# Kernel tuning notes

Hardware: AMD Instinct MI355X
Metric: run time of the kernel (lower is better)

## Reference

```python
import jax, jax.numpy as jnp
import numpy as np

N, E, F, H, G = 50000, 640000, 128, 128, 64


def setup_inputs() -> dict:
    key = jax.random.key(0)
    ks = jax.random.split(key, 10)
    x = jax.random.normal(ks[0], (N, F), dtype=jnp.float32)
    edge_index = jax.random.randint(ks[1], (2, E), 0, N)
    batch = jnp.sort(jax.random.randint(ks[2], (N,), 0, G))

    def glorot(k, shp):
        return jax.random.normal(k, shp, dtype=jnp.float32) * np.float32(1.0 / np.sqrt(shp[0]))

    W1 = glorot(ks[3], (F, H)); b1 = jnp.zeros((H,), jnp.float32)
    W2 = glorot(ks[4], (H, H)); b2 = jnp.zeros((H,), jnp.float32)
    W3 = glorot(ks[5], (H, H)); b3 = jnp.zeros((H,), jnp.float32)
    W4 = glorot(ks[6], (H, 2)); b4 = jnp.zeros((2,), jnp.float32)
    return {"x": x, "W1": W1, "b1": b1, "W2": W2, "b2": b2,
            "W3": W3, "b3": b3, "W4": W4, "b4": b4,
            "edge_index": edge_index, "batch": batch, "num_graphs": G}


def reference(x, W1, b1, W2, b2, W3, b3, W4, b4, edge_index, batch, num_graphs):
    n = x.shape[0]
    loop = jnp.arange(n, dtype=edge_index.dtype)
    src = jnp.concatenate([edge_index[0], loop])  # with self-loops (PyG GCNConv default)
    dst = jnp.concatenate([edge_index[1], loop])
    # symmetric degree normalization: D^{-1/2} (A+I) D^{-1/2}
    deg = jax.ops.segment_sum(jnp.ones_like(src, dtype=x.dtype), dst, num_segments=n)
    dinv = jnp.where(deg > 0, jax.lax.rsqrt(deg), 0.0)
    norm = (dinv[src] * dinv[dst])[:, None]  # [E+N, 1]

    def gcn_conv(h, W, b):
        m = h @ W                                   # transform first (F->H), then propagate
        agg = jax.ops.segment_sum(m[src] * norm, dst, num_segments=n)
        return agg + b

    h = jax.nn.relu(gcn_conv(x, W1, b1))
    h = jax.nn.relu(gcn_conv(h, W2, b2))
    g = jax.ops.segment_max(h, batch, num_segments=num_graphs)  # global_max_pool
    z = jax.nn.relu(g @ W3 + b3)                    # dropout is identity in eval
    logits = z @ W4 + b4
    return jax.nn.log_softmax(logits, axis=1)
```

## Files before the change

kernel.cpp:

```cpp
#include <hip/hip_runtime.h>
#include <hip/hip_bf16.h>
#include <math.h>

#define HDIM 128
#define SCAN_B 256
#define NBLK 256

typedef short bfrag __attribute__((ext_vector_type(8)));
typedef float f32x4 __attribute__((ext_vector_type(4)));

__device__ inline unsigned short f2bf_rne(float x) {
    unsigned u = __float_as_uint(x);
    u = (u + 0x7fffu + ((u >> 16) & 1u)) >> 16;
    return (unsigned short)u;
}
__device__ inline float bf_lo(unsigned u) { return __uint_as_float(u << 16); }
__device__ inline float bf_hi(unsigned u) { return __uint_as_float(u & 0xffff0000u); }
__device__ inline unsigned bf_pack(float lo, float hi) {
    return ((unsigned)f2bf_rne(hi) << 16) | (unsigned)f2bf_rne(lo);
}


__device__ inline void hist_body(int b, const int* __restrict__ dst,
                                 int* __restrict__ hist, int E, int chunk, int nbuck) {
    __shared__ int hl[256];
    int t = threadIdx.x;
    hl[t] = 0;
    __syncthreads();
    int start = b * chunk, end = min(E, start + chunk);
    for (int e = start + t; e < end; e += 256) atomicAdd(&hl[dst[e] >> 8], 1);
    __syncthreads();
    if (t < nbuck) hist[t * NBLK + b] = hl[t];
}

__device__ inline void wfrag_body(int b, const float* __restrict__ W1,
                                  const float* __restrict__ W2,
                                  unsigned short* __restrict__ w1h,
                                  unsigned short* __restrict__ w1l,
                                  unsigned short* __restrict__ w2h,
                                  unsigned short* __restrict__ w2l) {
    const float* W = (b < 64) ? W1 : W2;
    unsigned short* whi = (b < 64) ? w1h : w2h;
    unsigned short* wlo = (b < 64) ? w1l : w2l;
    int idx = (b & 63) * 256 + threadIdx.x;
    int k = idx >> 7;
    int n = idx & 127;
    int kt = k >> 5, q = (k >> 3) & 3, j = k & 7;
    int lm = n >> 3, nt = n & 7;
    int lane = q * 16 + lm;
    int o = ((kt * 8 + nt) * 64 + lane) * 8 + j;
    float x = W[idx];
    unsigned short hb = f2bf_rne(x);
    float hf = __uint_as_float(((unsigned)hb) << 16);
    unsigned short lb = f2bf_rne(x - hf);
    whi[o] = hb;
    wlo[o] = lb;
}

__device__ inline void scatter_body(int b, const int* __restrict__ srcv,
                                    const int* __restrict__ dstv,
                                    const int* __restrict__ hscan,
                                    int2* __restrict__ sorted,
                                    int E, int chunk, int nbuck) {
    __shared__ int cur[256];
    int t = threadIdx.x;
    if (t < nbuck) cur[t] = hscan[t * NBLK + b];
    __syncthreads();
    int start = b * chunk, end = min(E, start + chunk);
    for (int e = start + t; e < end; e += 256) {
        int d = dstv[e];
        int pos = atomicAdd(&cur[d >> 8], 1);
        sorted[pos] = make_int2(srcv[e], d);
    }
}

#define GBM 64
__device__ inline void gemm_f32_body(int b, const float* __restrict__ A,
                                     const unsigned short* __restrict__ whi,
                                     const unsigned short* __restrict__ wlo,
                                     unsigned short* __restrict__ C, int Nrows) {
    int tid = threadIdx.x;
    int w = tid >> 6, L = tid & 63;
    int lm = L & 15, lq = L >> 4;
    int row0 = b * GBM + w * 16;

    f32x4 acc[8];
#pragma unroll
    for (int nt = 0; nt < 8; ++nt) acc[nt] = (f32x4)(0.f);

#pragma unroll
    for (int kt = 0; kt < 4; ++kt) {
        int gr = row0 + lm;
        float4 v0 = make_float4(0.f, 0.f, 0.f, 0.f);
        float4 v1 = v0;
        if (gr < Nrows) {
            const float* p = &A[(size_t)gr * HDIM + kt * 32 + lq * 8];
            v0 = *(const float4*)p;
            v1 = *(const float4*)(p + 4);
        }
        float xv[8] = {v0.x, v0.y, v0.z, v0.w, v1.x, v1.y, v1.z, v1.w};
        bfrag ah, al;
#pragma unroll
        for (int j = 0; j < 8; ++j) {
            float x = xv[j];
            unsigned short hb = f2bf_rne(x);
            float hf = __uint_as_float(((unsigned)hb) << 16);
            unsigned short lb = f2bf_rne(x - hf);
            ah[j] = (short)hb;
            al[j] = (short)lb;
        }
#pragma unroll
        for (int nt = 0; nt < 8; ++nt) {
            int o = ((kt * 8 + nt) * 64 + L) * 8;
            bfrag wh = *(const bfrag*)&whi[o];
            bfrag wl = *(const bfrag*)&wlo[o];
            acc[nt] = __builtin_amdgcn_mfma_f32_16x16x32_bf16(ah, wh, acc[nt], 0, 0, 0);
            acc[nt] = __builtin_amdgcn_mfma_f32_16x16x32_bf16(al, wh, acc[nt], 0, 0, 0);
            acc[nt] = __builtin_amdgcn_mfma_f32_16x16x32_bf16(ah, wl, acc[nt], 0, 0, 0);
        }
    }

#pragma unroll
    for (int i = 0; i < 4; ++i) {
        int gr = row0 + lq * 4 + i;
        if (gr < Nrows) {
            bfrag e;
#pragma unroll
            for (int nt = 0; nt < 8; ++nt) e[nt] = (short)f2bf_rne(acc[nt][i]);
            *(bfrag*)&C[(size_t)gr * HDIM + lm * 8] = e;
        }
    }
}

__global__ __launch_bounds__(256) void mega1_kernel(const int* __restrict__ dst,
                                                    int* __restrict__ hist, int E,
                                                    int chunk, int nbuck,
                                                    const float* __restrict__ W1,
                                                    const float* __restrict__ W2,
                                                    unsigned short* __restrict__ w1h,
                                                    unsigned short* __restrict__ w1l,
                                                    unsigned short* __restrict__ w2h,
                                                    unsigned short* __restrict__ w2l) {
    int b = blockIdx.x;
    if (b < NBLK) hist_body(b, dst, hist, E, chunk, nbuck);
    else wfrag_body(b - NBLK, W1, W2, w1h, w1l, w2h, w2l);
}

__global__ __launch_bounds__(256) void mega3_kernel(const int* __restrict__ srcv,
                                                    const int* __restrict__ dstv,
                                                    const int* __restrict__ hscan,
                                                    int2* __restrict__ sorted,
                                                    int E, int chunk, int nbuck,
                                                    const float* __restrict__ A,
                                                    const unsigned short* __restrict__ whi,
                                                    const unsigned short* __restrict__ wlo,
                                                    unsigned short* __restrict__ C, int Nrows) {
    int b = blockIdx.x;
    if (b < NBLK) scatter_body(b, srcv, dstv, hscan, sorted, E, chunk, nbuck);
    else gemm_f32_body(b - NBLK, A, whi, wlo, C, Nrows);
}

__global__ __launch_bounds__(SCAN_B) void scan1_kernel(const int* __restrict__ in,
                                                       int* __restrict__ out,
                                                       int* __restrict__ sums, int n) {
    __shared__ int s[SCAN_B];
    int t = threadIdx.x;
    int idx = blockIdx.x * SCAN_B + t;
    int v = (idx < n) ? in[idx] : 0;
    s[t] = v;
    __syncthreads();
    for (int off = 1; off < SCAN_B; off <<= 1) {
        int x = (t >= off) ? s[t - off] : 0;
        __syncthreads();
        s[t] += x;
        __syncthreads();
    }
    if (idx < n) out[idx] = s[t];
    if (t == SCAN_B - 1) sums[blockIdx.x] = s[t];
}

__global__ __launch_bounds__(SCAN_B) void scan2_kernel(int* __restrict__ sums, int nb) {
    __shared__ int s[SCAN_B];
    int t = threadIdx.x;
    int v = (t < nb) ? sums[t] : 0;
    s[t] = v;
    __syncthreads();
    for (int off = 1; off < SCAN_B; off <<= 1) {
        int x = (t >= off) ? s[t - off] : 0;
        __syncthreads();
        s[t] += x;
        __syncthreads();
    }
    if (t < nb) sums[t] = s[t] - v;
}

__global__ __launch_bounds__(SCAN_B) void scan3_kernel(const int* __restrict__ in,
                                                       int* __restrict__ out,
                                                       const int* __restrict__ sums, int n) {
    int idx = blockIdx.x * SCAN_B + threadIdx.x;
    if (idx < n) out[idx] = out[idx] - in[idx] + sums[blockIdx.x];
}

__global__ __launch_bounds__(256) void csr_kernel(const int2* __restrict__ sorted,
                                                  const int* __restrict__ hscan,
                                                  int* __restrict__ rowstart,
                                                  float* __restrict__ dinv,
                                                  int* __restrict__ csr,
                                                  int N, int E, int nbuck) {
    __shared__ int cnt[256];
    __shared__ int s[256];
    __shared__ int cur[256];
    int b = blockIdx.x;
    int t = threadIdx.x;
    int start = hscan[b * NBLK];
    int end = (b + 1 < nbuck) ? hscan[(b + 1) * NBLK] : E;
    cnt[t] = 0;
    __syncthreads();
    for (int e = start + t; e < end; e += 256)
        atomicAdd(&cnt[sorted[e].y & 255], 1);
    __syncthreads();
    int v = cnt[t];
    s[t] = v;
    __syncthreads();
    for (int off = 1; off < 256; off <<= 1) {
        int x = (t >= off) ? s[t - off] : 0;
        __syncthreads();
        s[t] += x;
        __syncthreads();
    }
    int excl = s[t] - v;
    int node = b * 256 + t;
    if (node < N) {
        rowstart[node] = start + excl;
        dinv[node] = rsqrtf((float)(v + 1));
    }
    if (b == nbuck - 1 && t == 0) rowstart[N] = E;
    cur[t] = start + excl;
    __syncthreads();
    for (int e = start + t; e < end; e += 256) {
        int2 ed = sorted[e];
        int pos = atomicAdd(&cur[ed.y & 255], 1);
        csr[pos] = ed.x;
    }
}

__global__ __launch_bounds__(256) void gemm_bf16_kernel(
        const unsigned short* __restrict__ A16,
        const unsigned short* __restrict__ whi,
        const unsigned short* __restrict__ wlo,
        unsigned short* __restrict__ C, int Nrows) {
    int tid = threadIdx.x;
    int w = tid >> 6, L = tid & 63;
    int lm = L & 15, lq = L >> 4;
    int row0 = blockIdx.x * GBM + w * 16;

    f32x4 acc[8];
#pragma unroll
    for (int nt = 0; nt < 8; ++nt) acc[nt] = (f32x4)(0.f);

#pragma unroll
    for (int kt = 0; kt < 4; ++kt) {
        int gr = row0 + lm;
        bfrag ah = (bfrag)(short)0;
        if (gr < Nrows) ah = *(const bfrag*)&A16[(size_t)gr * HDIM + kt * 32 + lq * 8];
#pragma unroll
        for (int nt = 0; nt < 8; ++nt) {
            int o = ((kt * 8 + nt) * 64 + L) * 8;
            bfrag wh = *(const bfrag*)&whi[o];
            bfrag wl = *(const bfrag*)&wlo[o];
            acc[nt] = __builtin_amdgcn_mfma_f32_16x16x32_bf16(ah, wh, acc[nt], 0, 0, 0);
            acc[nt] = __builtin_amdgcn_mfma_f32_16x16x32_bf16(ah, wl, acc[nt], 0, 0, 0);
        }
    }

#pragma unroll
    for (int i = 0; i < 4; ++i) {
        int gr = row0 + lq * 4 + i;
        if (gr < Nrows) {
            bfrag e;
#pragma unroll
            for (int nt = 0; nt < 8; ++nt) e[nt] = (short)f2bf_rne(acc[nt][i]);
            *(bfrag*)&C[(size_t)gr * HDIM + lm * 8] = e;
        }
    }
}

#define QACC(UV, WT)                                   \
    acc[0] = fmaf(WT, bf_lo((UV).x), acc[0]);          \
    acc[1] = fmaf(WT, bf_hi((UV).x), acc[1]);          \
    acc[2] = fmaf(WT, bf_lo((UV).y), acc[2]);          \
    acc[3] = fmaf(WT, bf_hi((UV).y), acc[3]);          \
    acc[4] = fmaf(WT, bf_lo((UV).z), acc[4]);          \
    acc[5] = fmaf(WT, bf_hi((UV).z), acc[5]);          \
    acc[6] = fmaf(WT, bf_lo((UV).w), acc[6]);          \
    acc[7] = fmaf(WT, bf_hi((UV).w), acc[7]);

__device__ inline void qgather(const uint4* __restrict__ m4,
                               const int* __restrict__ csr,
                               const float* __restrict__ dinv,
                               int p, int pend, int t, float* acc) {
    for (; p + 4 <= pend; p += 4) {
        int s0 = csr[p], s1 = csr[p + 1], s2 = csr[p + 2], s3 = csr[p + 3];
        float w0 = dinv[s0], w1 = dinv[s1], w2 = dinv[s2], w3 = dinv[s3];
        uint4 u0 = m4[(size_t)s0 * 16 + t];
        uint4 u1 = m4[(size_t)s1 * 16 + t];
        uint4 u2 = m4[(size_t)s2 * 16 + t];
        uint4 u3 = m4[(size_t)s3 * 16 + t];
        QACC(u0, w0); QACC(u1, w1); QACC(u2, w2); QACC(u3, w3);
    }
    if (p + 2 <= pend) {
        int s0 = csr[p], s1 = csr[p + 1];
        float w0 = dinv[s0], w1 = dinv[s1];
        uint4 u0 = m4[(size_t)s0 * 16 + t];
        uint4 u1 = m4[(size_t)s1 * 16 + t];
        QACC(u0, w0); QACC(u1, w1);
        p += 2;
    }
    if (p < pend) {
        int s0 = csr[p];
        float w0 = dinv[s0];
        uint4 u0 = m4[(size_t)s0 * 16 + t];
        QACC(u0, w0);
    }
}

__global__ __launch_bounds__(256) void agg_kernel(const uint4* __restrict__ m4,
                                                  const int* __restrict__ rowstart,
                                                  const int* __restrict__ csr,
                                                  const float* __restrict__ dinv,
                                                  const float* __restrict__ bias,
                                                  uint4* __restrict__ out, int n) {
    int t = threadIdx.x & 15;
    int node = blockIdx.x * 16 + (threadIdx.x >> 4);
    if (node >= n) return;
    float dd = dinv[node];
    float acc[8];
    {
        uint4 u = m4[(size_t)node * 16 + t];
        acc[0] = dd * bf_lo(u.x); acc[1] = dd * bf_hi(u.x);
        acc[2] = dd * bf_lo(u.y); acc[3] = dd * bf_hi(u.y);
        acc[4] = dd * bf_lo(u.z); acc[5] = dd * bf_hi(u.z);
        acc[6] = dd * bf_lo(u.w); acc[7] = dd * bf_hi(u.w);
    }
    qgather(m4, csr, dinv, rowstart[node], rowstart[node + 1], t, acc);
    float4 b0 = *(const float4*)&bias[t * 8];
    float4 b1 = *(const float4*)&bias[t * 8 + 4];
    uint4 o;
    o.x = bf_pack(fmaxf(fmaf(dd, acc[0], b0.x), 0.f), fmaxf(fmaf(dd, acc[1], b0.y), 0.f));
    o.y = bf_pack(fmaxf(fmaf(dd, acc[2], b0.z), 0.f), fmaxf(fmaf(dd, acc[3], b0.w), 0.f));
    o.z = bf_pack(fmaxf(fmaf(dd, acc[4], b1.x), 0.f), fmaxf(fmaf(dd, acc[5], b1.y), 0.f));
    o.w = bf_pack(fmaxf(fmaf(dd, acc[6], b1.z), 0.f), fmaxf(fmaf(dd, acc[7], b1.w), 0.f));
    out[(size_t)node * 16 + t] = o;
}

__global__ __launch_bounds__(256) void agg_pool_kernel(const uint4* __restrict__ m4,
                                                       const int* __restrict__ rowstart,
                                                       const int* __restrict__ csr,
                                                       const float* __restrict__ dinv,
                                                       const float* __restrict__ bias,
                                                       const int* __restrict__ batch,
                                                       unsigned int* __restrict__ g, int n) {
    __shared__ float smx[16][HDIM];
    __shared__ int sgid[16];
    int t = threadIdx.x & 15;
    int nl = threadIdx.x >> 4;
    int node = blockIdx.x * 16 + nl;
    bool valid = node < n;
    if (valid) {
        float dd = dinv[node];
        float acc[8];
        uint4 u = m4[(size_t)node * 16 + t];
        acc[0] = dd * bf_lo(u.x); acc[1] = dd * bf_hi(u.x);
        acc[2] = dd * bf_lo(u.y); acc[3] = dd * bf_hi(u.y);
        acc[4] = dd * bf_lo(u.z); acc[5] = dd * bf_hi(u.z);
        acc[6] = dd * bf_lo(u.w); acc[7] = dd * bf_hi(u.w);
        qgather(m4, csr, dinv, rowstart[node], rowstart[node + 1], t, acc);
        float4 b0 = *(const float4*)&bias[t * 8];
        float4 b1 = *(const float4*)&bias[t * 8 + 4];
        float4 r0, r1;
        r0.x = fmaxf(fmaf(dd, acc[0], b0.x), 0.f);
        r0.y = fmaxf(fmaf(dd, acc[1], b0.y), 0.f);
        r0.z = fmaxf(fmaf(dd, acc[2], b0.z), 0.f);
        r0.w = fmaxf(fmaf(dd, acc[3], b0.w), 0.f);
        r1.x = fmaxf(fmaf(dd, acc[4], b1.x), 0.f);
        r1.y = fmaxf(fmaf(dd, acc[5], b1.y), 0.f);
        r1.z = fmaxf(fmaf(dd, acc[6], b1.z), 0.f);
        r1.w = fmaxf(fmaf(dd, acc[7], b1.w), 0.f);
        *(float4*)&smx[nl][t * 8] = r0;
        *(float4*)&smx[nl][t * 8 + 4] = r1;
    }
    if (t == 0) sgid[nl] = valid ? batch[node] : -1;
    __syncthreads();
    if (threadIdx.x < HDIM) {
        int c = threadIdx.x;
        int curg = -1;
        float run = 0.f;
#pragma unroll
        for (int r = 0; r < 16; ++r) {
            int gg = sgid[r];
            if (gg < 0) continue;
            if (gg != curg) {
                if (curg >= 0) atomicMax(&g[curg * HDIM + c], __float_as_uint(run));
                curg = gg;
                run = smx[r][c];
            } else {
                run = fmaxf(run, smx[r][c]);
            }
        }
        if (curg >= 0) atomicMax(&g[curg * HDIM + c], __float_as_uint(run));
    }
}

__global__ __launch_bounds__(128) void mlp_kernel(const unsigned int* __restrict__ gbits,
                                                  const float* __restrict__ W3,
                                                  const float* __restrict__ b3,
                                                  const float* __restrict__ W4,
                                                  const float* __restrict__ b4,
                                                  float* __restrict__ out) {
    __shared__ float gs[HDIM];
    __shared__ float r0[HDIM];
    __shared__ float r1[HDIM];
    int j = threadIdx.x;
    int b = blockIdx.x;
    gs[j] = __uint_as_float(gbits[b * HDIM + j]);
    __syncthreads();
    float acc = b3[j];
#pragma unroll 8
    for (int k = 0; k < HDIM; ++k) acc = fmaf(gs[k], W3[k * HDIM + j], acc);
    float z = fmaxf(acc, 0.f);
    r0[j] = z * W4[j * 2 + 0];
    r1[j] = z * W4[j * 2 + 1];
    __syncthreads();
    for (int off = 64; off > 0; off >>= 1) {
        if (j < off) {
            r0[j] += r0[j + off];
            r1[j] += r1[j + off];
        }
        __syncthreads();
    }
    if (j == 0) {
        float l0 = r0[0] + b4[0];
        float l1 = r1[0] + b4[1];
        float mx = fmaxf(l0, l1);
        float lse = mx + logf(expf(l0 - mx) + expf(l1 - mx));
        out[b * 2 + 0] = l0 - lse;
        out[b * 2 + 1] = l1 - lse;
    }
}

extern "C" void kernel_launch(void* const* d_in, const int* in_sizes, int n_in,
                              void* d_out, int out_size, void* d_ws, size_t ws_size,
                              hipStream_t stream) {
    const float* x  = (const float*)d_in[0];
    const float* W1 = (const float*)d_in[1];
    const float* b1 = (const float*)d_in[2];
    const float* W2 = (const float*)d_in[3];
    const float* b2 = (const float*)d_in[4];
    const float* W3 = (const float*)d_in[5];
    const float* b3 = (const float*)d_in[6];
    const float* W4 = (const float*)d_in[7];
    const float* b4 = (const float*)d_in[8];
    const int* ei    = (const int*)d_in[9];
    const int* batch = (const int*)d_in[10];

    const int N = in_sizes[0] / HDIM;
    const int E = in_sizes[9] / 2;
    const int G = out_size / 2;
    const int* src = ei;
    const int* dst = ei + E;

    const int nbuck = (N + 255) >> 8;
    const int nscan = nbuck * NBLK;
    const int chunk = (E + NBLK - 1) / NBLK;

    const int Nr = ((N + 63) / 64) * 64;
    char* wsb = (char*)d_ws;
    size_t o = 0;
    unsigned int* g = (unsigned int*)(wsb + o); o += (size_t)G * HDIM * 4;
    size_t zero_bytes = o;
    int* hist = (int*)(wsb + o);           o += (size_t)nscan * 4;
    int* hscan = (int*)(wsb + o);          o += (size_t)nscan * 4;
    int* sums = (int*)(wsb + o);           o += 256 * 4;
    int* rowstart = (int*)(wsb + o);       o += (size_t)(Nr + 64) * 4;
    float* dinv = (float*)(wsb + o);       o += (size_t)Nr * 4;
    int2* sorted = (int2*)(wsb + o);       o += (size_t)E * 8;
    int* csr = (int*)(wsb + o);            o += (size_t)E * 4;
    unsigned short* wf1h = (unsigned short*)(wsb + o); o += (size_t)HDIM * HDIM * 2;
    unsigned short* wf1l = (unsigned short*)(wsb + o); o += (size_t)HDIM * HDIM * 2;
    unsigned short* wf2h = (unsigned short*)(wsb + o); o += (size_t)HDIM * HDIM * 2;
    unsigned short* wf2l = (unsigned short*)(wsb + o); o += (size_t)HDIM * HDIM * 2;
    unsigned short* m = (unsigned short*)(wsb + o);    o += (size_t)Nr * HDIM * 2;
    unsigned short* h = (unsigned short*)(wsb + o);    o += (size_t)Nr * HDIM * 2;
    (void)ws_size; (void)n_in;

    (void)hipMemsetAsync(d_ws, 0, zero_bytes, stream);

    int sblocks = (nscan + SCAN_B - 1) / SCAN_B;
    int gemm_blocks = (N + GBM - 1) / GBM;
    int agg_blocks = (N + 15) / 16;

    mega1_kernel<<<NBLK + 128, 256, 0, stream>>>(dst, hist, E, chunk, nbuck,
                                                 W1, W2, wf1h, wf1l, wf2h, wf2l);
    scan1_kernel<<<sblocks, SCAN_B, 0, stream>>>(hist, hscan, sums, nscan);
    scan2_kernel<<<1, SCAN_B, 0, stream>>>(sums, sblocks);
    scan3_kernel<<<sblocks, SCAN_B, 0, stream>>>(hist, hscan, sums, nscan);
    mega3_kernel<<<NBLK + gemm_blocks, 256, 0, stream>>>(src, dst, hscan, sorted,
                                                         E, chunk, nbuck,
                                                         x, wf1h, wf1l, m, N);
    csr_kernel<<<nbuck, 256, 0, stream>>>(sorted, hscan, rowstart, dinv, csr, N, E, nbuck);
    agg_kernel<<<agg_blocks, 256, 0, stream>>>((const uint4*)m, rowstart, csr,
                                               dinv, b1, (uint4*)h, N);
    gemm_bf16_kernel<<<gemm_blocks, 256, 0, stream>>>(h, wf2h, wf2l, m, N);
    agg_pool_kernel<<<agg_blocks, 256, 0, stream>>>((const uint4*)m, rowstart, csr,
                                                    dinv, b2, batch, g, N);
    mlp_kernel<<<G, 128, 0, stream>>>(g, W3, b3, W4, b4, (float*)d_out);
}
```

Measured before the change: 205.7 us.

## Fuse layer-1 aggregation with layer-2 GEMM and widen gather unroll to 8

Merges the first aggregation kernel and the second bf16 MFMA GEMM into one kernel. Each block aggregates 16 nodes into shared memory, then multiplies that tile by W2 with MFMA, so the intermediate h no longer round-trips through global memory and one launch disappears. The edge-gather loop is also unrolled to 8 neighbours to put more loads in flight. In exchange the kernel uses more shared memory, adds two barriers, and runs a small 16-row GEMM per block whose weight fragments are reloaded from global memory by every block.

```diff
diff --git a/kernel.cpp b/kernel.cpp
--- a/kernel.cpp
+++ b/kernel.cpp
@@ -244,47 +244,6 @@
     }
 }
 
-__global__ __launch_bounds__(256) void gemm_bf16_kernel(
-        const unsigned short* __restrict__ A16,
-        const unsigned short* __restrict__ whi,
-        const unsigned short* __restrict__ wlo,
-        unsigned short* __restrict__ C, int Nrows) {
-    int tid = threadIdx.x;
-    int w = tid >> 6, L = tid & 63;
-    int lm = L & 15, lq = L >> 4;
-    int row0 = blockIdx.x * GBM + w * 16;
-
-    f32x4 acc[8];
-#pragma unroll
-    for (int nt = 0; nt < 8; ++nt) acc[nt] = (f32x4)(0.f);
-
-#pragma unroll
-    for (int kt = 0; kt < 4; ++kt) {
-        int gr = row0 + lm;
-        bfrag ah = (bfrag)(short)0;
-        if (gr < Nrows) ah = *(const bfrag*)&A16[(size_t)gr * HDIM + kt * 32 + lq * 8];
-#pragma unroll
-        for (int nt = 0; nt < 8; ++nt) {
-            int o = ((kt * 8 + nt) * 64 + L) * 8;
-            bfrag wh = *(const bfrag*)&whi[o];
-            bfrag wl = *(const bfrag*)&wlo[o];
-            acc[nt] = __builtin_amdgcn_mfma_f32_16x16x32_bf16(ah, wh, acc[nt], 0, 0, 0);
-            acc[nt] = __builtin_amdgcn_mfma_f32_16x16x32_bf16(ah, wl, acc[nt], 0, 0, 0);
-        }
-    }
-
-#pragma unroll
-    for (int i = 0; i < 4; ++i) {
-        int gr = row0 + lq * 4 + i;
-        if (gr < Nrows) {
-            bfrag e;
-#pragma unroll
-            for (int nt = 0; nt < 8; ++nt) e[nt] = (short)f2bf_rne(acc[nt][i]);
-            *(bfrag*)&C[(size_t)gr * HDIM + lm * 8] = e;
-        }
-    }
-}
-
 #define QACC(UV, WT)                                   \
     acc[0] = fmaf(WT, bf_lo((UV).x), acc[0]);          \
     acc[1] = fmaf(WT, bf_hi((UV).x), acc[1]);          \
@@ -299,7 +258,23 @@
                                const int* __restrict__ csr,
                                const float* __restrict__ dinv,
                                int p, int pend, int t, float* acc) {
-    for (; p + 4 <= pend; p += 4) {
+    for (; p + 8 <= pend; p += 8) {
+        int s0 = csr[p], s1 = csr[p + 1], s2 = csr[p + 2], s3 = csr[p + 3];
+        int s4 = csr[p + 4], s5 = csr[p + 5], s6 = csr[p + 6], s7 = csr[p + 7];
+        float w0 = dinv[s0], w1 = dinv[s1], w2 = dinv[s2], w3 = dinv[s3];
+        float w4 = dinv[s4], w5 = dinv[s5], w6 = dinv[s6], w7 = dinv[s7];
+        uint4 u0 = m4[(size_t)s0 * 16 + t];
+        uint4 u1 = m4[(size_t)s1 * 16 + t];
+        uint4 u2 = m4[(size_t)s2 * 16 + t];
+        uint4 u3 = m4[(size_t)s3 * 16 + t];
+        uint4 u4 = m4[(size_t)s4 * 16 + t];
+        uint4 u5 = m4[(size_t)s5 * 16 + t];
+        uint4 u6 = m4[(size_t)s6 * 16 + t];
+        uint4 u7 = m4[(size_t)s7 * 16 + t];
+        QACC(u0, w0); QACC(u1, w1); QACC(u2, w2); QACC(u3, w3);
+        QACC(u4, w4); QACC(u5, w5); QACC(u6, w6); QACC(u7, w7);
+    }
+    if (p + 4 <= pend) {
         int s0 = csr[p], s1 = csr[p + 1], s2 = csr[p + 2], s3 = csr[p + 3];
         float w0 = dinv[s0], w1 = dinv[s1], w2 = dinv[s2], w3 = dinv[s3];
         uint4 u0 = m4[(size_t)s0 * 16 + t];
@@ -307,6 +282,7 @@
         uint4 u2 = m4[(size_t)s2 * 16 + t];
         uint4 u3 = m4[(size_t)s3 * 16 + t];
         QACC(u0, w0); QACC(u1, w1); QACC(u2, w2); QACC(u3, w3);
+        p += 4;
     }
     if (p + 2 <= pend) {
         int s0 = csr[p], s1 = csr[p + 1];
@@ -324,33 +300,77 @@
     }
 }
 
-__global__ __launch_bounds__(256) void agg_kernel(const uint4* __restrict__ m4,
-                                                  const int* __restrict__ rowstart,
-                                                  const int* __restrict__ csr,
-                                                  const float* __restrict__ dinv,
-                                                  const float* __restrict__ bias,
-                                                  uint4* __restrict__ out, int n) {
+__global__ __launch_bounds__(256) void agg_gemm_kernel(
+        const uint4* __restrict__ m4,
+        const int* __restrict__ rowstart,
+        const int* __restrict__ csr,
+        const float* __restrict__ dinv,
+        const float* __restrict__ bias,
+        const unsigned short* __restrict__ whi,
+        const unsigned short* __restrict__ wlo,
+        uint4* __restrict__ out_m, int n) {
+    __shared__ unsigned short hbuf[16][HDIM + 8];
+    __shared__ float cbuf[16][HDIM + 4];
     int t = threadIdx.x & 15;
-    int node = blockIdx.x * 16 + (threadIdx.x >> 4);
-    if (node >= n) return;
-    float dd = dinv[node];
-    float acc[8];
-    {
+    int nl = threadIdx.x >> 4;
+    int node = blockIdx.x * 16 + nl;
+
+    unsigned short hv[8] = {0, 0, 0, 0, 0, 0, 0, 0};
+    if (node < n) {
+        float dd = dinv[node];
+        float acc[8];
         uint4 u = m4[(size_t)node * 16 + t];
         acc[0] = dd * bf_lo(u.x); acc[1] = dd * bf_hi(u.x);
         acc[2] = dd * bf_lo(u.y); acc[3] = dd * bf_hi(u.y);
         acc[4] = dd * bf_lo(u.z); acc[5] = dd * bf_hi(u.z);
         acc[6] = dd * bf_lo(u.w); acc[7] = dd * bf_hi(u.w);
-    }
-    qgather(m4, csr, dinv, rowstart[node], rowstart[node + 1], t, acc);
-    float4 b0 = *(const float4*)&bias[t * 8];
-    float4 b1 = *(const float4*)&bias[t * 8 + 4];
-    uint4 o;
-    o.x = bf_pack(fmaxf(fmaf(dd, acc[0], b0.x), 0.f), fmaxf(fmaf(dd, acc[1], b0.y), 0.f));
-    o.y = bf_pack(fmaxf(fmaf(dd, acc[2], b0.z), 0.f), fmaxf(fmaf(dd, acc[3], b0.w), 0.f));
-    o.z = bf_pack(fmaxf(fmaf(dd, acc[4], b1.x), 0.f), fmaxf(fmaf(dd, acc[5], b1.y), 0.f));
-    o.w = bf_pack(fmaxf(fmaf(dd, acc[6], b1.z), 0.f), fmaxf(fmaf(dd, acc[7], b1.w), 0.f));
-    out[(size_t)node * 16 + t] = o;
+        qgather(m4, csr, dinv, rowstart[node], rowstart[node + 1], t, acc);
+        float4 b0 = *(const float4*)&bias[t * 8];
+        float4 b1 = *(const float4*)&bias[t * 8 + 4];
+        float bb[8] = {b0.x, b0.y, b0.z, b0.w, b1.x, b1.y, b1.z, b1.w};
+#pragma unroll
+        for (int j = 0; j < 8; ++j)
+            hv[j] = f2bf_rne(fmaxf(fmaf(dd, acc[j], bb[j]), 0.f));
+    }
+    *(uint4*)&hbuf[nl][t * 8] = *(uint4*)hv;
+    __syncthreads();
+
+    int w = threadIdx.x >> 6, L = threadIdx.x & 63;
+    int lm = L & 15, lq = L >> 4;
+    f32x4 acc2[2];
+    acc2[0] = (f32x4)(0.f);
+    acc2[1] = (f32x4)(0.f);
+#pragma unroll
+    for (int kt = 0; kt < 4; ++kt) {
+        bfrag a = *(const bfrag*)&hbuf[lm][kt * 32 + lq * 8];
+#pragma unroll
+        for (int q2 = 0; q2 < 2; ++q2) {
+            int nt = w * 2 + q2;
+            int o = ((kt * 8 + nt) * 64 + L) * 8;
+            bfrag wh = *(const bfrag*)&whi[o];
+            bfrag wl = *(const bfrag*)&wlo[o];
+            acc2[q2] = __builtin_amdgcn_mfma_f32_16x16x32_bf16(a, wh, acc2[q2], 0, 0, 0);
+            acc2[q2] = __builtin_amdgcn_mfma_f32_16x16x32_bf16(a, wl, acc2[q2], 0, 0, 0);
+        }
+    }
+#pragma unroll
+    for (int q2 = 0; q2 < 2; ++q2) {
+        int nt = w * 2 + q2;
+#pragma unroll
+        for (int i = 0; i < 4; ++i) cbuf[lq * 4 + i][lm * 8 + nt] = acc2[q2][i];
+    }
+    __syncthreads();
+
+    if (node < n) {
+        float4 r0 = *(const float4*)&cbuf[nl][t * 8];
+        float4 r1 = *(const float4*)&cbuf[nl][t * 8 + 4];
+        unsigned short ev[8];
+        ev[0] = f2bf_rne(r0.x); ev[1] = f2bf_rne(r0.y);
+        ev[2] = f2bf_rne(r0.z); ev[3] = f2bf_rne(r0.w);
+        ev[4] = f2bf_rne(r1.x); ev[5] = f2bf_rne(r1.y);
+        ev[6] = f2bf_rne(r1.z); ev[7] = f2bf_rne(r1.w);
+        out_m[(size_t)node * 16 + t] = *(uint4*)ev;
+    }
 }
 
 __global__ __launch_bounds__(256) void agg_pool_kernel(const uint4* __restrict__ m4,
@@ -490,7 +510,7 @@
     unsigned short* wf2h = (unsigned short*)(wsb + o); o += (size_t)HDIM * HDIM * 2;
     unsigned short* wf2l = (unsigned short*)(wsb + o); o += (size_t)HDIM * HDIM * 2;
     unsigned short* m = (unsigned short*)(wsb + o);    o += (size_t)Nr * HDIM * 2;
-    unsigned short* h = (unsigned short*)(wsb + o);    o += (size_t)Nr * HDIM * 2;
+    unsigned short* m2 = (unsigned short*)(wsb + o);   o += (size_t)Nr * HDIM * 2;
     (void)ws_size; (void)n_in;
 
     (void)hipMemsetAsync(d_ws, 0, zero_bytes, stream);
@@ -508,10 +528,10 @@
                                                          E, chunk, nbuck,
                                                          x, wf1h, wf1l, m, N);
     csr_kernel<<<nbuck, 256, 0, stream>>>(sorted, hscan, rowstart, dinv, csr, N, E, nbuck);
-    agg_kernel<<<agg_blocks, 256, 0, stream>>>((const uint4*)m, rowstart, csr,
-                                               dinv, b1, (uint4*)h, N);
-    gemm_bf16_kernel<<<gemm_blocks, 256, 0, stream>>>(h, wf2h, wf2l, m, N);
-    agg_pool_kernel<<<agg_blocks, 256, 0, stream>>>((const uint4*)m, rowstart, csr,
+    agg_gemm_kernel<<<agg_blocks, 256, 0, stream>>>((const uint4*)m, rowstart, csr,
+                                                    dinv, b1, wf2h, wf2l,
+                                                    (uint4*)m2, N);
+    agg_pool_kernel<<<agg_blocks, 256, 0, stream>>>((const uint4*)m2, rowstart, csr,
                                                     dinv, b2, batch, g, N);
     mlp_kernel<<<G, 128, 0, stream>>>(g, W3, b3, W4, b4, (float*)d_out);
 }
```

After: 201.7 us. No clear change (-2.0%).
